# Performance work log

Measured on AMD Instinct MI355X. Metric: run time of the kernel, lower is better.

## Reference

```python
import jax, jax.numpy as jnp
import numpy as np

B, T, C = 4, 2048, 1024
H = 16
D = C // H  # head_size = 64


def setup_inputs() -> dict:
    key = jax.random.key(0)
    ks = jax.random.split(key, 5)
    s = 0.02
    return {
        "x": jax.random.normal(ks[0], (B, T, C), dtype=jnp.float32),
        "Wq": jax.random.normal(ks[1], (C, C), dtype=jnp.float32) * s,
        "Wk": jax.random.normal(ks[2], (C, C), dtype=jnp.float32) * s,
        "Wv": jax.random.normal(ks[3], (C, C), dtype=jnp.float32) * s,
        "Wp": jax.random.normal(ks[4], (C, C), dtype=jnp.float32) * s,
        "bp": jnp.zeros((C,), dtype=jnp.float32),
    }


def reference(x, Wq, Wk, Wv, Wp, bp):
    Bq, Tq, Cq = x.shape
    # torch Linear: y = x @ W.T ; split into heads [B, H, T, D]
    def split(y):
        return y.reshape(Bq, Tq, H, D).transpose(0, 2, 1, 3)
    q = split(x @ Wq.T)
    k = split(x @ Wk.T)
    v = split(x @ Wv.T)
    # NOTE: original scales by C**-0.5 (full n_embed), not head_size**-0.5
    scale = Cq ** (-0.5)
    att = jnp.einsum('bhqd,bhkd->bhqk', q, k) * scale  # [B,H,T,T]
    causal = jnp.tril(jnp.ones((Tq, Tq), dtype=bool))
    att = jnp.where(causal[None, None, :, :], att, -jnp.inf)
    att = jax.nn.softmax(att, axis=-1)
    out = jnp.einsum('bhqk,bhkd->bhqd', att, v)  # [B,H,T,D]
    out = out.transpose(0, 2, 1, 3).reshape(Bq, Tq, Cq)
    return out @ Wp.T + bp
```

## Files before the change

### kernel.cpp

```cpp
#include <hip/hip_runtime.h>
#include <cstdint>
#include <cstddef>

typedef __attribute__((ext_vector_type(8))) __bf16 bf16x8;
typedef __attribute__((ext_vector_type(4))) __bf16 bf16x4;
typedef __attribute__((ext_vector_type(4))) float f32x4;
typedef __attribute__((ext_vector_type(16))) float f32x16;
typedef __attribute__((ext_vector_type(4))) unsigned uint4v;

#define B_ 4
#define T_ 2048
#define C_ 1024
#define H_ 16
#define D_ 64
#define NTILES_ (T_ / 32)
#define TILE_ELEMS_ 2048
#define BH_STRIDE_ ((size_t)NTILES_ * TILE_ELEMS_)

__device__ __forceinline__ float fexp2(float x) {
#if __has_builtin(__builtin_amdgcn_exp2f)
  return __builtin_amdgcn_exp2f(x);
#else
  return __expf(x * 0.69314718f);
#endif
}

__global__ __launch_bounds__(256) void castk(const float* __restrict__ in,
                                             __bf16* __restrict__ out, int n) {
  int i = (blockIdx.x * blockDim.x + threadIdx.x) * 4;
  if (i >= n) return;
  float4 f = *reinterpret_cast<const float4*>(in + i);
  bf16x4 o;
  o[0] = (__bf16)f.x; o[1] = (__bf16)f.y; o[2] = (__bf16)f.z; o[3] = (__bf16)f.w;
  *reinterpret_cast<bf16x4*>(out + i) = o;
}

__device__ __forceinline__ void gload_lds16(const __bf16* g, __bf16* lds) {
  __builtin_amdgcn_global_load_lds(
      (const __attribute__((address_space(1))) void*)g,
      (__attribute__((address_space(3))) void*)lds, 16, 0, 0);
}

template <typename OUTT, bool BIAS>
__device__ __forceinline__ void gemm_bt_body(const __bf16* __restrict__ A,
                                             const __bf16* __restrict__ Bt,
                                             OUTT* __restrict__ Cp,
                                             const float* __restrict__ bias,
                                             int M, int N, int K) {
  constexpr int BK = 64;
  __shared__ __bf16 As[128 * BK];
  __shared__ __bf16 Bs[128 * BK];
  const int tid = threadIdx.x;
  const int w = tid >> 6, l = tid & 63;
  const int wr = w >> 1, wc = w & 1;
  const int lr = l & 15, lg = l >> 4;
  const int m0 = blockIdx.y * 128, n0 = blockIdx.x * 128;
  const int srow = l >> 3, scol = (l & 7) * 8;

  f32x4 acc[4][4] = {};

  for (int k0 = 0; k0 < K; k0 += BK) {
#pragma unroll
    for (int it = 0; it < 4; ++it) {
      const int c = w * 4 + it;
      gload_lds16(A + (size_t)(m0 + 8 * c + srow) * K + k0 + scol, As + c * 512);
      gload_lds16(Bt + (size_t)(n0 + 8 * c + srow) * K + k0 + scol, Bs + c * 512);
    }
    __syncthreads();
    bf16x8 af[4][2], bfv[4][2];
#pragma unroll
    for (int m = 0; m < 4; ++m)
#pragma unroll
      for (int kk = 0; kk < 2; ++kk)
        af[m][kk] = *reinterpret_cast<const bf16x8*>(As + (wr * 64 + m * 16 + lr) * BK + kk * 32 + lg * 8);
#pragma unroll
    for (int n = 0; n < 4; ++n)
#pragma unroll
      for (int kk = 0; kk < 2; ++kk)
        bfv[n][kk] = *reinterpret_cast<const bf16x8*>(Bs + (wc * 64 + n * 16 + lr) * BK + kk * 32 + lg * 8);
#pragma unroll
    for (int kk = 0; kk < 2; ++kk)
#pragma unroll
      for (int m = 0; m < 4; ++m)
#pragma unroll
        for (int n = 0; n < 4; ++n)
          acc[m][n] = __builtin_amdgcn_mfma_f32_16x16x32_bf16(af[m][kk], bfv[n][kk], acc[m][n], 0, 0, 0);
    __syncthreads();
  }
#pragma unroll
  for (int m = 0; m < 4; ++m)
#pragma unroll
    for (int n = 0; n < 4; ++n) {
      const int col = n0 + wc * 64 + n * 16 + lr;
      float bv = 0.f;
      if (BIAS) bv = bias[col];
#pragma unroll
      for (int j = 0; j < 4; ++j) {
        const int row = m0 + wr * 64 + m * 16 + lg * 4 + j;
        Cp[(size_t)row * N + col] = (OUTT)(acc[m][n][j] + bv);
      }
    }
}

__global__ __launch_bounds__(256) void gemm_proj(const __bf16* __restrict__ ao,
    const __bf16* __restrict__ wp, float* __restrict__ out, const float* __restrict__ bp) {
  gemm_bt_body<float, true>(ao, wp, out, bp, B_ * T_, C_, C_);
}


#define STAGE_A(BUFO, KT, HH)                                                         \
  do {                                                                                \
    const __bf16* s0_ = Agp + (size_t)(m0 + (HH) * 128 + srow) * 1024 + (KT) * 64 + sswz; \
    gload_lds16(s0_, LDSb + (BUFO) + (HH) * 8192 + w * 1024);                         \
    gload_lds16(s0_ + 8 * 1024, LDSb + (BUFO) + (HH) * 8192 + w * 1024 + 512);        \
  } while (0)
#define STAGE_B(BUFO, KT, HH)                                                         \
  do {                                                                                \
    const __bf16* s0_ = Bgp + (size_t)(n0 + (HH) * 128 + srow) * 1024 + (KT) * 64 + sswz; \
    gload_lds16(s0_, LDSb + 32768 + (BUFO) + (HH) * 8192 + w * 1024);                 \
    gload_lds16(s0_ + 8 * 1024, LDSb + 32768 + (BUFO) + (HH) * 8192 + w * 1024 + 512);\
  } while (0)
#define RD_A(M, KK) (*reinterpret_cast<const bf16x8*>(                                \
    LDSb + bufo + (wr * 128 + (M) * 16 + lr) * 64 + (((KK) * 32 + lg * 8) ^ ((lr & 7) * 8))))
#define RD_B(N, KK) (*reinterpret_cast<const bf16x8*>(                                \
    LDSb + 32768 + bufo + (wc * 64 + (N) * 16 + lr) * 64 + (((KK) * 32 + lg * 8) ^ ((lr & 7) * 8))))

__global__ __launch_bounds__(512, 2) void gemm_qkv8(
    const __bf16* __restrict__ Agp, const __bf16* __restrict__ Bgp,
    __bf16* __restrict__ qf, __bf16* __restrict__ kf, __bf16* __restrict__ vf) {
  __shared__ __bf16 LDSb[65536];
  const int tid = threadIdx.x;
  const int w = tid >> 6, l = tid & 63;
  const int wr = w >> 2, wc = w & 3;
  const int lr = l & 15, lg = l >> 4;
  int lin = blockIdx.y * 12 + blockIdx.x;
  lin = (lin & 7) * 48 + (lin >> 3);
  const int bx = lin % 12, by = lin / 12;
  const int m0 = by * 256, n0 = bx * 256;
  const int srow = w * 16 + (l >> 3);
  const int sswz = ((l & 7) ^ ((l >> 3) & 7)) * 8;

  f32x4 acc[8][4] = {};
  bf16x8 afl[4][2], bfl[2][2], bfh[2][2];

  STAGE_A(0, 0, 0); STAGE_A(0, 0, 1);
  STAGE_B(0, 0, 0); STAGE_B(0, 0, 1);
  __builtin_amdgcn_sched_barrier(0);
  asm volatile("s_waitcnt vmcnt(0)" ::: "memory");
  __builtin_amdgcn_s_barrier();
  __builtin_amdgcn_sched_barrier(0);

  for (int t = 0; t < 16; ++t) {
    const int bufo = (t & 1) * 16384;
    const int nbo = ((t + 1) & 1) * 16384;
    const bool st = t < 15;
#pragma unroll
    for (int m = 0; m < 4; ++m) { afl[m][0] = RD_A(m, 0); afl[m][1] = RD_A(m, 1); }
    bfl[0][0] = RD_B(0, 0); bfl[0][1] = RD_B(0, 1);
    bfl[1][0] = RD_B(1, 0); bfl[1][1] = RD_B(1, 1);
    if (st) STAGE_A(nbo, t + 1, 0);
    __builtin_amdgcn_s_setprio(1);
#pragma unroll
    for (int kk = 0; kk < 2; ++kk)
#pragma unroll
      for (int m = 0; m < 4; ++m) {
        acc[m][0] = __builtin_amdgcn_mfma_f32_16x16x32_bf16(afl[m][kk], bfl[0][kk], acc[m][0], 0, 0, 0);
        acc[m][1] = __builtin_amdgcn_mfma_f32_16x16x32_bf16(afl[m][kk], bfl[1][kk], acc[m][1], 0, 0, 0);
      }
    __builtin_amdgcn_s_setprio(0);
    __builtin_amdgcn_s_barrier();
    bfh[0][0] = RD_B(2, 0); bfh[0][1] = RD_B(2, 1);
    bfh[1][0] = RD_B(3, 0); bfh[1][1] = RD_B(3, 1);
    if (st) STAGE_A(nbo, t + 1, 1);
    __builtin_amdgcn_s_setprio(1);
#pragma unroll
    for (int kk = 0; kk < 2; ++kk)
#pragma unroll
      for (int m = 0; m < 4; ++m) {
        acc[m][2] = __builtin_amdgcn_mfma_f32_16x16x32_bf16(afl[m][kk], bfh[0][kk], acc[m][2], 0, 0, 0);
        acc[m][3] = __builtin_amdgcn_mfma_f32_16x16x32_bf16(afl[m][kk], bfh[1][kk], acc[m][3], 0, 0, 0);
      }
    __builtin_amdgcn_s_setprio(0);
    __builtin_amdgcn_s_barrier();
#pragma unroll
    for (int m = 0; m < 4; ++m) { afl[m][0] = RD_A(m + 4, 0); afl[m][1] = RD_A(m + 4, 1); }
    if (st) STAGE_B(nbo, t + 1, 0);
    __builtin_amdgcn_s_setprio(1);
#pragma unroll
    for (int kk = 0; kk < 2; ++kk)
#pragma unroll
      for (int m = 0; m < 4; ++m) {
        acc[m + 4][0] = __builtin_amdgcn_mfma_f32_16x16x32_bf16(afl[m][kk], bfl[0][kk], acc[m + 4][0], 0, 0, 0);
        acc[m + 4][1] = __builtin_amdgcn_mfma_f32_16x16x32_bf16(afl[m][kk], bfl[1][kk], acc[m + 4][1], 0, 0, 0);
      }
    __builtin_amdgcn_s_setprio(0);
    __builtin_amdgcn_s_barrier();
    if (st) STAGE_B(nbo, t + 1, 1);
    __builtin_amdgcn_s_setprio(1);
#pragma unroll
    for (int kk = 0; kk < 2; ++kk)
#pragma unroll
      for (int m = 0; m < 4; ++m) {
        acc[m + 4][2] = __builtin_amdgcn_mfma_f32_16x16x32_bf16(afl[m][kk], bfh[0][kk], acc[m + 4][2], 0, 0, 0);
        acc[m + 4][3] = __builtin_amdgcn_mfma_f32_16x16x32_bf16(afl[m][kk], bfh[1][kk], acc[m + 4][3], 0, 0, 0);
      }
    __builtin_amdgcn_s_setprio(0);
    __builtin_amdgcn_sched_barrier(0);
    asm volatile("s_waitcnt vmcnt(0)" ::: "memory");
    __builtin_amdgcn_s_barrier();
    __builtin_amdgcn_sched_barrier(0);
  }

  __bf16* wl = LDSb + w * 8192;
  const int colb = n0 + wc * 64;
  const int mat = colb >> 10;
  const int h = (colb >> 6) & 15;
  const int b = m0 >> 11;
#pragma unroll
  for (int m = 0; m < 8; ++m) {
    const int rt = m >> 1;
#pragma unroll
    for (int n = 0; n < 4; ++n) {
      const int d = n * 16 + lr;
#pragma unroll
      for (int j = 0; j < 4; ++j) {
        const int rowloc = (m & 1) * 16 + lg * 4 + j;
        int off;
        if (mat < 2)
          off = ((d >> 4) & 3) * 512 + ((d >> 3) & 1) * 256 + rowloc * 8 + (d & 7);
        else
          off = (d >> 5) * 1024 + ((rowloc >> 4) & 1) * 512 + ((rowloc >> 3) & 1) * 256 +
                (d & 31) * 8 + (rowloc & 7);
        wl[rt * 2048 + off] = (__bf16)acc[m][n][j];
      }
    }
  }
  __bf16* dstbase = (mat == 0 ? qf : mat == 1 ? kf : vf) + (size_t)(b * 16 + h) * BH_STRIDE_;
  const int rt0 = ((m0 + wr * 128) >> 5) & 63;
#pragma unroll
  for (int rt = 0; rt < 4; ++rt)
#pragma unroll
    for (int c = 0; c < 4; ++c) {
      const bf16x8 vchunk = *reinterpret_cast<const bf16x8*>(wl + rt * 2048 + c * 512 + l * 8);
      *reinterpret_cast<bf16x8*>(dstbase + (size_t)(rt0 + rt) * TILE_ELEMS_ + c * 512 + l * 8) = vchunk;
    }
}

__device__ __forceinline__ unsigned pk2(float a, float b) {
  const unsigned short ua = __builtin_bit_cast(unsigned short, (__bf16)a);
  const unsigned short ub = __builtin_bit_cast(unsigned short, (__bf16)b);
  return (unsigned)ua | ((unsigned)ub << 16);
}

#define LOADKV(SFX, TT)                                                          \
  do {                                                                           \
    const __bf16* kp_ = kfb + (size_t)(TT) * TILE_ELEMS_ + lx8;                  \
    k##SFX##0 = *reinterpret_cast<const bf16x8*>(kp_);                           \
    k##SFX##1 = *reinterpret_cast<const bf16x8*>(kp_ + 512);                     \
    k##SFX##2 = *reinterpret_cast<const bf16x8*>(kp_ + 1024);                    \
    k##SFX##3 = *reinterpret_cast<const bf16x8*>(kp_ + 1536);                    \
    const __bf16* vp_ = vfb + (size_t)(TT) * TILE_ELEMS_ + lx8;                  \
    v##SFX##0 = *reinterpret_cast<const bf16x8*>(vp_);                           \
    v##SFX##1 = *reinterpret_cast<const bf16x8*>(vp_ + 512);                     \
    v##SFX##2 = *reinterpret_cast<const bf16x8*>(vp_ + 1024);                    \
    v##SFX##3 = *reinterpret_cast<const bf16x8*>(vp_ + 1536);                    \
  } while (0)

#define TILE(SFX, MASKED)                                                        \
  do {                                                                           \
    f32x16 s = {};                                                               \
    __builtin_amdgcn_s_setprio(1);                                               \
    s = __builtin_amdgcn_mfma_f32_32x32x16_bf16(k##SFX##0, qf[0], s, 0, 0, 0);   \
    s = __builtin_amdgcn_mfma_f32_32x32x16_bf16(k##SFX##1, qf[1], s, 0, 0, 0);   \
    s = __builtin_amdgcn_mfma_f32_32x32x16_bf16(k##SFX##2, qf[2], s, 0, 0, 0);   \
    s = __builtin_amdgcn_mfma_f32_32x32x16_bf16(k##SFX##3, qf[3], s, 0, 0, 0);   \
    __builtin_amdgcn_s_setprio(0);                                               \
    float sv[16];                                                                \
    _Pragma("unroll") for (int r = 0; r < 16; ++r) sv[r] = s[r];                 \
    if (MASKED) {                                                                \
      _Pragma("unroll") for (int r = 0; r < 16; ++r) {                           \
        const int kvloc = (r & 3) + 8 * (r >> 2) + 4 * hi;                       \
        sv[r] = (kvloc <= lane31) ? sv[r] : -1e30f;                              \
      }                                                                          \
    }                                                                            \
    _Pragma("unroll") for (int r = 0; r < 16; ++r)                               \
      sv[r] = fexp2(sv[r] * K2);                                                 \
    unsigned pwv[8];                                                             \
    _Pragma("unroll") for (int ks = 0; ks < 2; ++ks) {                           \
      const unsigned X0 = pk2(sv[ks * 8 + 0], sv[ks * 8 + 1]);                   \
      const unsigned X1 = pk2(sv[ks * 8 + 2], sv[ks * 8 + 3]);                   \
      const unsigned Y0 = pk2(sv[ks * 8 + 4], sv[ks * 8 + 5]);                   \
      const unsigned Y1 = pk2(sv[ks * 8 + 6], sv[ks * 8 + 7]);                   \
      const unsigned sX0 = __shfl_xor(X0, 32);                                   \
      const unsigned sX1 = __shfl_xor(X1, 32);                                   \
      const unsigned sY0 = __shfl_xor(Y0, 32);                                   \
      const unsigned sY1 = __shfl_xor(Y1, 32);                                   \
      pwv[ks * 4 + 0] = hi ? sY0 : X0;                                           \
      pwv[ks * 4 + 1] = hi ? sY1 : X1;                                           \
      pwv[ks * 4 + 2] = hi ? Y0 : sX0;                                           \
      pwv[ks * 4 + 3] = hi ? Y1 : sX1;                                           \
    }                                                                            \
    const uint4v u0 = {pwv[0], pwv[1], pwv[2], pwv[3]};                          \
    const uint4v u1 = {pwv[4], pwv[5], pwv[6], pwv[7]};                          \
    const bf16x8 pf0 = __builtin_bit_cast(bf16x8, u0);                           \
    const bf16x8 pf1 = __builtin_bit_cast(bf16x8, u1);                           \
    __builtin_amdgcn_s_setprio(1);                                               \
    acc0 = __builtin_amdgcn_mfma_f32_32x32x16_bf16(v##SFX##0, pf0, acc0, 0, 0, 0); \
    acc0 = __builtin_amdgcn_mfma_f32_32x32x16_bf16(v##SFX##1, pf1, acc0, 0, 0, 0); \
    acc1 = __builtin_amdgcn_mfma_f32_32x32x16_bf16(v##SFX##2, pf0, acc1, 0, 0, 0); \
    acc1 = __builtin_amdgcn_mfma_f32_32x32x16_bf16(v##SFX##3, pf1, acc1, 0, 0, 0); \
    __builtin_amdgcn_s_setprio(0);                                               \
    float b8[8];                                                                 \
    _Pragma("unroll") for (int r = 0; r < 8; ++r) b8[r] = sv[2 * r] + sv[2 * r + 1]; \
    _Pragma("unroll") for (int r = 0; r < 4; ++r) b8[r] = b8[2 * r] + b8[2 * r + 1]; \
    l_run += (b8[0] + b8[1]) + (b8[2] + b8[3]);                                  \
  } while (0)

__global__ __launch_bounds__(256) void attn_fwd(const __bf16* __restrict__ qfr,
                                                const __bf16* __restrict__ kfr,
                                                const __bf16* __restrict__ vfr,
                                                __bf16* __restrict__ ao) {
  const int tid = threadIdx.x;
  const int w = tid >> 6, l = tid & 63;
  const int lane31 = l & 31, hi = l >> 5;
  const int bh = blockIdx.y;
  const int b = bh >> 4;
  const int qx = blockIdx.x * 4 + w;
  const size_t rowbase = (size_t)b * T_;
  const int hoff = (bh & 15) * D_;
  const int lx8 = l * 8;
  const __bf16* qfb = qfr + (size_t)bh * BH_STRIDE_;
  const __bf16* kfb = kfr + (size_t)bh * BH_STRIDE_;
  const __bf16* vfb = vfr + (size_t)bh * BH_STRIDE_;
  const float K2 = 0.04508422f;

  for (int phase = 0; phase < 2; ++phase) {
    const int qg = (phase ? 63 - qx : qx) * 32;
    const int ntiles = (qg >> 5) + 1;

    bf16x8 qf[4];
    {
      const __bf16* qp = qfb + (size_t)(qg >> 5) * TILE_ELEMS_ + lx8;
#pragma unroll
      for (int t4 = 0; t4 < 4; ++t4) qf[t4] = *reinterpret_cast<const bf16x8*>(qp + t4 * 512);
    }

    f32x16 acc0 = {};
    f32x16 acc1 = {};
    float l_run = 0.f;

    bf16x8 kA0, kA1, kA2, kA3, vA0, vA1, vA2, vA3;
    bf16x8 kB0, kB1, kB2, kB3, vB0, vB1, vB2, vB3;

    LOADKV(A, 0);
    int t = 0;
    for (; t + 1 < ntiles; ++t) {
      if ((t & 1) == 0) { LOADKV(B, t + 1); TILE(A, false); }
      else              { LOADKV(A, t + 1); TILE(B, false); }
    }
    if ((t & 1) == 0) TILE(A, true);
    else              TILE(B, true);

    l_run += __shfl_xor(l_run, 32);

    const float rl = 1.0f / l_run;
    __bf16* op = ao + (rowbase + qg + lane31) * C_ + hoff + hi * 4;
#pragma unroll
    for (int dblk = 0; dblk < 2; ++dblk)
#pragma unroll
      for (int qd = 0; qd < 4; ++qd) {
        bf16x4 ov;
#pragma unroll
        for (int j = 0; j < 4; ++j) {
          const float av = (dblk == 0) ? acc0[qd * 4 + j] : acc1[qd * 4 + j];
          ov[j] = (__bf16)(av * rl);
        }
        *reinterpret_cast<bf16x4*>(op + dblk * 32 + qd * 8) = ov;
      }
  }
}

extern "C" void kernel_launch(void* const* d_in, const int* in_sizes, int n_in,
                              void* d_out, int out_size, void* d_ws, size_t ws_size,
                              hipStream_t stream) {
  const float* x  = (const float*)d_in[0];
  const float* Wq = (const float*)d_in[1];
  const float* Wk = (const float*)d_in[2];
  const float* Wv = (const float*)d_in[3];
  const float* Wp = (const float*)d_in[4];
  const float* bp = (const float*)d_in[5];
  float* out = (float*)d_out;

  const int NX = B_ * T_ * C_;
  const int NW = C_ * C_;

  __bf16* xb  = (__bf16*)d_ws;
  __bf16* wqb = xb + NX;
  __bf16* wkb = wqb + NW;
  __bf16* wvb = wkb + NW;
  __bf16* wpb = wvb + NW;
  __bf16* qf  = wpb + NW;
  __bf16* kf  = qf + NX;
  __bf16* vf  = kf + NX;
  __bf16* aob = xb;

  castk<<<NX / 1024, 256, 0, stream>>>(x, xb, NX);
  castk<<<NW / 1024, 256, 0, stream>>>(Wq, wqb, NW);
  castk<<<NW / 1024, 256, 0, stream>>>(Wk, wkb, NW);
  castk<<<NW / 1024, 256, 0, stream>>>(Wv, wvb, NW);
  castk<<<NW / 1024, 256, 0, stream>>>(Wp, wpb, NW);

  gemm_qkv8<<<dim3(12, 32), 512, 0, stream>>>(xb, wqb, qf, kf, vf);
  attn_fwd<<<dim3(8, B_ * H_), 256, 0, stream>>>(qf, kf, vf, aob);
  gemm_proj<<<dim3(C_ / 128, (B_ * T_) / 128), 256, 0, stream>>>(aob, wpb, out, bp);
}
```

Baseline: 180.9 us.

## Split attention KV range across two waves, fold scale into Q, fuse casts

Each query tile's KV loop is now split between two waves, doubling waves per block to 512 threads. The second wave's partial accumulators and row sum are merged through LDS before normalisation. This works without max-rescaling because the softmax is computed without a running max. The softmax scale is folded into the Q projection epilogue, which removes a multiply per score, and the five cast launches are merged into one kernel. Risks are extra LDS traffic, two block barriers per phase, and a small bf16 rounding change from pre-scaling Q.

After: 181.5 us. No clear change (+0.3%).

```diff
diff --git a/kernel.cpp b/kernel.cpp
--- a/kernel.cpp
+++ b/kernel.cpp
@@ -25,14 +25,24 @@
 #endif
 }
 
-__global__ __launch_bounds__(256) void castk(const float* __restrict__ in,
-                                             __bf16* __restrict__ out, int n) {
-  int i = (blockIdx.x * blockDim.x + threadIdx.x) * 4;
-  if (i >= n) return;
-  float4 f = *reinterpret_cast<const float4*>(in + i);
+__global__ __launch_bounds__(256) void castall(
+    const float* __restrict__ x, const float* __restrict__ wq, const float* __restrict__ wk,
+    const float* __restrict__ wv, const float* __restrict__ wp,
+    __bf16* __restrict__ xb, __bf16* __restrict__ wqb, __bf16* __restrict__ wkb,
+    __bf16* __restrict__ wvb, __bf16* __restrict__ wpb) {
+  const int bid = blockIdx.x;
+  const float* src;
+  __bf16* dst;
+  if (bid < 8192)       { src = x  + (size_t)bid * 1024;           dst = xb  + (size_t)bid * 1024; }
+  else if (bid < 9216)  { src = wq + (size_t)(bid - 8192) * 1024;  dst = wqb + (size_t)(bid - 8192) * 1024; }
+  else if (bid < 10240) { src = wk + (size_t)(bid - 9216) * 1024;  dst = wkb + (size_t)(bid - 9216) * 1024; }
+  else if (bid < 11264) { src = wv + (size_t)(bid - 10240) * 1024; dst = wvb + (size_t)(bid - 10240) * 1024; }
+  else                  { src = wp + (size_t)(bid - 11264) * 1024; dst = wpb + (size_t)(bid - 11264) * 1024; }
+  const int i = threadIdx.x * 4;
+  float4 f = *reinterpret_cast<const float4*>(src + i);
   bf16x4 o;
   o[0] = (__bf16)f.x; o[1] = (__bf16)f.y; o[2] = (__bf16)f.z; o[3] = (__bf16)f.w;
-  *reinterpret_cast<bf16x4*>(out + i) = o;
+  *reinterpret_cast<bf16x4*>(dst + i) = o;
 }
 
 __device__ __forceinline__ void gload_lds16(const __bf16* g, __bf16* lds) {
@@ -106,7 +116,6 @@
     const __bf16* __restrict__ wp, float* __restrict__ out, const float* __restrict__ bp) {
   gemm_bt_body<float, true>(ao, wp, out, bp, B_ * T_, C_, C_);
 }
-
 
 #define STAGE_A(BUFO, KT, HH)                                                         \
   do {                                                                                \
@@ -216,6 +225,7 @@
   const int mat = colb >> 10;
   const int h = (colb >> 6) & 15;
   const int b = m0 >> 11;
+  const float qsc = (mat == 0) ? 0.04508422f : 1.0f;
 #pragma unroll
   for (int m = 0; m < 8; ++m) {
     const int rt = m >> 1;
@@ -231,7 +241,7 @@
         else
           off = (d >> 5) * 1024 + ((rowloc >> 4) & 1) * 512 + ((rowloc >> 3) & 1) * 256 +
                 (d & 31) * 8 + (rowloc & 7);
-        wl[rt * 2048 + off] = (__bf16)acc[m][n][j];
+        wl[rt * 2048 + off] = (__bf16)(acc[m][n][j] * qsc);
       }
     }
   }
@@ -283,8 +293,7 @@
         sv[r] = (kvloc <= lane31) ? sv[r] : -1e30f;                              \
       }                                                                          \
     }                                                                            \
-    _Pragma("unroll") for (int r = 0; r < 16; ++r)                               \
-      sv[r] = fexp2(sv[r] * K2);                                                 \
+    _Pragma("unroll") for (int r = 0; r < 16; ++r) sv[r] = fexp2(sv[r]);         \
     unsigned pwv[8];                                                             \
     _Pragma("unroll") for (int ks = 0; ks < 2; ++ks) {                           \
       const unsigned X0 = pk2(sv[ks * 8 + 0], sv[ks * 8 + 1]);                   \
@@ -316,27 +325,34 @@
     l_run += (b8[0] + b8[1]) + (b8[2] + b8[3]);                                  \
   } while (0)
 
-__global__ __launch_bounds__(256) void attn_fwd(const __bf16* __restrict__ qfr,
+__global__ __launch_bounds__(512) void attn_fwd(const __bf16* __restrict__ qfr,
                                                 const __bf16* __restrict__ kfr,
                                                 const __bf16* __restrict__ vfr,
                                                 __bf16* __restrict__ ao) {
+  __shared__ float Pls[4 * 64 * 34];
   const int tid = threadIdx.x;
   const int w = tid >> 6, l = tid & 63;
+  const int p = w >> 1, hf = w & 1;
   const int lane31 = l & 31, hi = l >> 5;
   const int bh = blockIdx.y;
   const int b = bh >> 4;
-  const int qx = blockIdx.x * 4 + w;
+  const int qx = blockIdx.x * 4 + p;
   const size_t rowbase = (size_t)b * T_;
   const int hoff = (bh & 15) * D_;
   const int lx8 = l * 8;
   const __bf16* qfb = qfr + (size_t)bh * BH_STRIDE_;
   const __bf16* kfb = kfr + (size_t)bh * BH_STRIDE_;
   const __bf16* vfb = vfr + (size_t)bh * BH_STRIDE_;
-  const float K2 = 0.04508422f;
+  float* pb = Pls + p * (64 * 34) + l * 34;
 
   for (int phase = 0; phase < 2; ++phase) {
     const int qg = (phase ? 63 - qx : qx) * 32;
     const int ntiles = (qg >> 5) + 1;
+    const int nh = ntiles >> 1;
+    const int tb = hf ? nh : 0;
+    const int te = hf ? ntiles : nh;
+    const int nt = te - tb;
+    const bool dm = (hf == 1);
 
     bf16x8 qf[4];
     {
@@ -352,31 +368,44 @@
     bf16x8 kA0, kA1, kA2, kA3, vA0, vA1, vA2, vA3;
     bf16x8 kB0, kB1, kB2, kB3, vB0, vB1, vB2, vB3;
 
-    LOADKV(A, 0);
-    int t = 0;
-    for (; t + 1 < ntiles; ++t) {
-      if ((t & 1) == 0) { LOADKV(B, t + 1); TILE(A, false); }
-      else              { LOADKV(A, t + 1); TILE(B, false); }
-    }
-    if ((t & 1) == 0) TILE(A, true);
-    else              TILE(B, true);
-
-    l_run += __shfl_xor(l_run, 32);
-
-    const float rl = 1.0f / l_run;
-    __bf16* op = ao + (rowbase + qg + lane31) * C_ + hoff + hi * 4;
-#pragma unroll
-    for (int dblk = 0; dblk < 2; ++dblk)
-#pragma unroll
-      for (int qd = 0; qd < 4; ++qd) {
-        bf16x4 ov;
-#pragma unroll
-        for (int j = 0; j < 4; ++j) {
-          const float av = (dblk == 0) ? acc0[qd * 4 + j] : acc1[qd * 4 + j];
-          ov[j] = (__bf16)(av * rl);
+    if (nt > 0) {
+      LOADKV(A, tb);
+      int i = 0;
+      for (; i + 1 < nt; ++i) {
+        if ((i & 1) == 0) { LOADKV(B, tb + i + 1); TILE(A, false); }
+        else              { LOADKV(A, tb + i + 1); TILE(B, false); }
+      }
+      if ((i & 1) == 0) TILE(A, dm);
+      else              TILE(B, dm);
+    }
+
+    if (hf) {
+#pragma unroll
+      for (int r = 0; r < 16; ++r) { pb[r] = acc0[r]; pb[16 + r] = acc1[r]; }
+      pb[32] = l_run;
+    }
+    __syncthreads();
+    if (!hf) {
+#pragma unroll
+      for (int r = 0; r < 16; ++r) { acc0[r] += pb[r]; acc1[r] += pb[16 + r]; }
+      l_run += pb[32];
+      l_run += __shfl_xor(l_run, 32);
+      const float rl = 1.0f / l_run;
+      __bf16* op = ao + (rowbase + qg + lane31) * C_ + hoff + hi * 4;
+#pragma unroll
+      for (int dblk = 0; dblk < 2; ++dblk)
+#pragma unroll
+        for (int qd = 0; qd < 4; ++qd) {
+          bf16x4 ov;
+#pragma unroll
+          for (int j = 0; j < 4; ++j) {
+            const float av = (dblk == 0) ? acc0[qd * 4 + j] : acc1[qd * 4 + j];
+            ov[j] = (__bf16)(av * rl);
+          }
+          *reinterpret_cast<bf16x4*>(op + dblk * 32 + qd * 8) = ov;
         }
-        *reinterpret_cast<bf16x4*>(op + dblk * 32 + qd * 8) = ov;
-      }
+    }
+    __syncthreads();
   }
 }
 
@@ -404,13 +433,9 @@
   __bf16* vf  = kf + NX;
   __bf16* aob = xb;
 
-  castk<<<NX / 1024, 256, 0, stream>>>(x, xb, NX);
-  castk<<<NW / 1024, 256, 0, stream>>>(Wq, wqb, NW);
-  castk<<<NW / 1024, 256, 0, stream>>>(Wk, wkb, NW);
-  castk<<<NW / 1024, 256, 0, stream>>>(Wv, wvb, NW);
-  castk<<<NW / 1024, 256, 0, stream>>>(Wp, wpb, NW);
+  castall<<<12288, 256, 0, stream>>>(x, Wq, Wk, Wv, Wp, xb, wqb, wkb, wvb, wpb);
 
   gemm_qkv8<<<dim3(12, 32), 512, 0, stream>>>(xb, wqb, qf, kf, vf);
-  attn_fwd<<<dim3(8, B_ * H_), 256, 0, stream>>>(qf, kf, vf, aob);
+  attn_fwd<<<dim3(8, B_ * H_), 512, 0, stream>>>(qf, kf, vf, aob);
   gemm_proj<<<dim3(C_ / 128, (B_ * T_) / 128), 256, 0, stream>>>(aob, wpb, out, bp);
 }
```
